# Kernel optimization log

Hardware: AMD Instinct MI355X
Metric: run time of the kernel (lower is better)

Reference implementation:

```python
import jax, jax.numpy as jnp
import numpy as np

B, T_IN, F, U = 4096, 256, 32, 64
OUT_STEPS = 24


def _lstm_step(x, h, c, W, R, b):
    # Keras LSTMCell: gates z = x@W + h@R + b, split as [i, f, g, o]
    z = x @ W + h @ R + b  # [B, 4U]
    i, f, g, o = jnp.split(z, 4, axis=-1)
    i = jax.nn.sigmoid(i)
    f = jax.nn.sigmoid(f)
    g = jnp.tanh(g)
    o = jax.nn.sigmoid(o)
    c_new = f * c + i * g
    h_new = o * jnp.tanh(c_new)
    return h_new, c_new


def setup_inputs() -> dict:
    key = jax.random.key(0)
    ks = jax.random.split(key, 9)
    s_in = 1.0 / np.sqrt(F)
    s_hid = 1.0 / np.sqrt(U)
    return {
        "inputs": jax.random.normal(ks[0], (B, T_IN, F), jnp.float32),
        "W1": jax.random.normal(ks[1], (F, 4 * U), jnp.float32) * s_in,
        "U1": jax.random.normal(ks[2], (U, 4 * U), jnp.float32) * s_hid,
        "b1": jnp.zeros((4 * U,), jnp.float32),
        "W2": jax.random.normal(ks[3], (F, 4 * U), jnp.float32) * s_in,
        "U2": jax.random.normal(ks[4], (U, 4 * U), jnp.float32) * s_hid,
        "b2": jnp.zeros((4 * U,), jnp.float32),
        "Wd": jax.random.normal(ks[5], (U, F), jnp.float32) * s_hid,
        "bd": jnp.zeros((F,), jnp.float32),
    }


def reference(inputs, W1, U1, b1, W2, U2, b2, Wd, bd):
    batch = inputs.shape[0]
    units = U1.shape[0]
    h0 = jnp.zeros((batch, units), inputs.dtype)
    c0 = jnp.zeros((batch, units), inputs.dtype)

    # ---- warmup: run lstm_cell_warmup over the input sequence ----
    def warm_step(carry, x_t):
        h, c = carry
        h, c = _lstm_step(x_t, h, c, W1, U1, b1)
        return (h, c), None

    (h, c), _ = jax.lax.scan(warm_step, (h0, c0), jnp.swapaxes(inputs, 0, 1))
    pred0 = h @ Wd + bd  # [B, F]

    def dec_step(carry, _):
        pred, h, c = carry
        h, c = _lstm_step(pred, h, c, W2, U2, b2)
        pred = h @ Wd + bd
        return (pred, h, c), pred

    _, preds_rest = jax.lax.scan(dec_step, (pred0, h, c), None, length=OUT_STEPS - 1)
    preds = jnp.concatenate([pred0[None], preds_rest], axis=0)  # [T_out, B, F]
    return jnp.transpose(preds, (1, 0, 2))  # [B, T_out, F]
```

## Files before the change

kernel.cpp:

```cpp
#include <hip/hip_runtime.h>
#include <math.h>

#define T_STEPS 256
#define Fdim 32
#define Udim 64
#define G4 256
#define OUT_STEPS 24
#define ROWS 16
#define NBLK 256
#define NTHR 512
#define HBS 72
#define CHUNK 16
#define NCHUNK 16
#define LOG2E 1.4426950408889634f

typedef __attribute__((ext_vector_type(8))) short short8;
typedef __attribute__((ext_vector_type(4))) float f32x4;

__device__ __forceinline__ short f2bf(float f) {
    union { float f; unsigned u; } v; v.f = f;
    unsigned r = v.u + 0x7FFFu + ((v.u >> 16) & 1u);
    return (short)(r >> 16);
}
__device__ __forceinline__ float bf2f(short s) {
    union { unsigned u; float f; } v; v.u = ((unsigned)(unsigned short)s) << 16;
    return v.f;
}
__device__ __forceinline__ float frcp(float v) { return __builtin_amdgcn_rcpf(v); }
__device__ __forceinline__ float fexp2(float v) { return __builtin_amdgcn_exp2f(v); }

__device__ __forceinline__ unsigned pkbf(float lo, float hi) {
    unsigned r;
    asm("v_cvt_pk_bf16_f32 %0, %1, %2" : "=v"(r) : "v"(lo), "v"(hi));
    return r;
}

__device__ __forceinline__ float cell_h(const f32x4 a, float& cst) {
    float A  = fexp2(-a[0]);
    float Bv = fexp2(a[2]);
    float rf = frcp(1.0f + fexp2(-a[1]));
    float ig = (Bv - 1.0f) * frcp((1.0f + A) * (1.0f + Bv));
    cst = fmaf(cst, rf, ig);
    float C  = fexp2(-a[3]);
    float D  = fexp2(2.0f * LOG2E * cst);
    return (D - 1.0f) * frcp((1.0f + C) * (1.0f + D));
}

#define BAR() asm volatile("s_waitcnt lgkmcnt(0)\n\ts_barrier" ::: "memory")

#define MFMA __builtin_amdgcn_mfma_f32_16x16x32_bf16

__global__ __launch_bounds__(NTHR, 2)
void lstm_v10(const float* __restrict__ x,
              const float* __restrict__ W1, const float* __restrict__ U1, const float* __restrict__ b1,
              const float* __restrict__ W2, const float* __restrict__ U2, const float* __restrict__ b2,
              const float* __restrict__ Wd, const float* __restrict__ bd,
              float* __restrict__ out)
{
    __shared__ __align__(16) short hb[2][ROWS][HBS];
    __shared__ __align__(16) short xs[CHUNK][ROWS][HBS];

    const int tid = threadIdx.x;
    const int l   = tid & 63;
    const int w   = tid >> 6;
    const int q   = l >> 4;
    const int m   = l & 15;
    const int brow = blockIdx.x * ROWS;

    const int f4  = tid & 7;
    const int tt  = (tid >> 3) & 15;
    const int xr0 = tid >> 7;
    float4 pf[4];
#pragma unroll
    for (int i = 0; i < 4; ++i)
        pf[i] = *(const float4*)&x[((size_t)(brow + xr0 + 4 * i) * T_STEPS + tt) * Fdim + f4 * 4];

    short8 wa1[2][3], wa2[2][3];
    f32x4 bs1[2], bs2[2];
#pragma unroll
    for (int nt = 0; nt < 2; ++nt) {
        const int unit_a = w * 8 + (m >> 2) * 2 + nt;
        const int gate_a = m & 3;
        const int col = gate_a * 64 + unit_a;
        const float sA = (gate_a == 2) ? 2.0f * LOG2E : LOG2E;
#pragma unroll
        for (int kt = 0; kt < 3; ++kt) {
            short8 fa, fb;
#pragma unroll
            for (int j = 0; j < 8; ++j) {
                const int k = kt * 32 + q * 8 + j;
                float v1 = (k < Udim) ? U1[k * G4 + col] : W1[(k - Udim) * G4 + col];
                float v2 = (k < Udim) ? U2[k * G4 + col] : W2[(k - Udim) * G4 + col];
                fa[j] = f2bf(v1 * sA);
                fb[j] = f2bf(v2 * sA);
            }
            wa1[nt][kt] = fa;
            wa2[nt][kt] = fb;
        }
        const int unit_d = w * 8 + q * 2 + nt;
#pragma unroll
        for (int g = 0; g < 4; ++g) {
            const float sD = (g == 2) ? 2.0f * LOG2E : LOG2E;
            bs1[nt][g] = b1[g * 64 + unit_d] * sD;
            bs2[nt][g] = b2[g * 64 + unit_d] * sD;
        }
    }

    short8 wdh[2], wdlo[2];
    f32x4 bdC;
    {
        const int wsel = (w < 2) ? w : 0;
#pragma unroll
        for (int kt = 0; kt < 2; ++kt) {
            short8 fh, fl;
#pragma unroll
            for (int j = 0; j < 8; ++j) {
                const float v = Wd[(kt * 32 + q * 8 + j) * Fdim + 16 * wsel + m];
                const short hi = f2bf(v);
                fh[j] = hi;
                fl[j] = f2bf(v - bf2f(hi));
            }
            wdh[kt] = fh;
            wdlo[kt] = fl;
        }
#pragma unroll
        for (int g = 0; g < 4; ++g) bdC[g] = bd[16 * wsel + q * 4 + g];
    }

    const int hw = w * 8 + q * 2;
    for (int idx = tid; idx < 2 * ROWS * HBS; idx += NTHR) ((short*)hb)[idx] = 0;
    float cst[2] = {0.f, 0.f};

    for (int c = 0; c < NCHUNK; ++c) {
#pragma unroll
        for (int i = 0; i < 4; ++i) {
            uint2 pk;
            pk.x = pkbf(pf[i].x, pf[i].y);
            pk.y = pkbf(pf[i].z, pf[i].w);
            *(uint2*)&xs[tt][xr0 + 4 * i][f4 * 4] = pk;
        }
        if (c + 1 < NCHUNK) {
#pragma unroll
            for (int i = 0; i < 4; ++i)
                pf[i] = *(const float4*)&x[((size_t)(brow + xr0 + 4 * i) * T_STEPS + ((c + 1) * CHUNK + tt)) * Fdim + f4 * 4];
        }
        BAR();

        short8 xf[CHUNK];
#pragma unroll
        for (int t = 0; t < CHUNK; ++t)
            xf[t] = *(const short8*)&xs[t][m][q * 8];

#pragma unroll
        for (int t2 = 0; t2 < CHUNK; ++t2) {
            const int p = t2 & 1;

            const short8 b0  = *(const short8*)&hb[p][m][q * 8];
            const short8 b1v = *(const short8*)&hb[p][m][32 + q * 8];

            f32x4 a0 = MFMA(wa1[0][2], xf[t2], bs1[0], 0, 0, 0);
            f32x4 a1 = MFMA(wa1[1][2], xf[t2], bs1[1], 0, 0, 0);
            a0 = MFMA(wa1[0][0], b0, a0, 0, 0, 0);
            a1 = MFMA(wa1[1][0], b0, a1, 0, 0, 0);
            a0 = MFMA(wa1[0][1], b1v, a0, 0, 0, 0);
            a1 = MFMA(wa1[1][1], b1v, a1, 0, 0, 0);

            const float h0 = cell_h(a0, cst[0]);
            const float h1 = cell_h(a1, cst[1]);
            *(unsigned*)&hb[1 - p][m][hw] = pkbf(h0, h1);
            BAR();
        }
    }

    short8 b0p = *(const short8*)&hb[0][m][q * 8];
    short8 b1p = *(const short8*)&hb[0][m][32 + q * 8];
    if (w < 2) {
        f32x4 pz = MFMA(wdh[0], b0p, bdC, 0, 0, 0);
        pz = MFMA(wdh[1], b1p, pz, 0, 0, 0);
        pz = MFMA(wdlo[0], b0p, pz, 0, 0, 0);
        pz = MFMA(wdlo[1], b1p, pz, 0, 0, 0);
        *(f32x4*)&out[(size_t)(brow + m) * (OUT_STEPS * Fdim) + 16 * w + q * 4] = pz;
        uint2 fp;
        fp.x = pkbf(pz[0], pz[1]);
        fp.y = pkbf(pz[2], pz[3]);
        *(uint2*)&xs[0][m][16 * w + q * 4] = fp;
    }
    BAR();

    int dp = 0;
    for (int s = 1; s < OUT_STEPS; ++s) {
        const short8 b2v = *(const short8*)&xs[0][m][q * 8];

        f32x4 a0 = MFMA(wa2[0][0], b0p, bs2[0], 0, 0, 0);
        f32x4 a1 = MFMA(wa2[1][0], b0p, bs2[1], 0, 0, 0);
        a0 = MFMA(wa2[0][1], b1p, a0, 0, 0, 0);
        a1 = MFMA(wa2[1][1], b1p, a1, 0, 0, 0);
        a0 = MFMA(wa2[0][2], b2v, a0, 0, 0, 0);
        a1 = MFMA(wa2[1][2], b2v, a1, 0, 0, 0);

        const float h0 = cell_h(a0, cst[0]);
        const float h1 = cell_h(a1, cst[1]);
        *(unsigned*)&hb[1 - dp][m][hw] = pkbf(h0, h1);
        BAR();

        b0p = *(const short8*)&hb[1 - dp][m][q * 8];
        b1p = *(const short8*)&hb[1 - dp][m][32 + q * 8];
        if (w < 2) {
            f32x4 pz = MFMA(wdh[0], b0p, bdC, 0, 0, 0);
            pz = MFMA(wdh[1], b1p, pz, 0, 0, 0);
            pz = MFMA(wdlo[0], b0p, pz, 0, 0, 0);
            pz = MFMA(wdlo[1], b1p, pz, 0, 0, 0);
            *(f32x4*)&out[(size_t)(brow + m) * (OUT_STEPS * Fdim) + s * Fdim + 16 * w + q * 4] = pz;
            uint2 fp;
            fp.x = pkbf(pz[0], pz[1]);
            fp.y = pkbf(pz[2], pz[3]);
            *(uint2*)&xs[0][m][16 * w + q * 4] = fp;
        }
        BAR();
        dp = 1 - dp;
    }
}

extern "C" void kernel_launch(void* const* d_in, const int* in_sizes, int n_in,
                              void* d_out, int out_size, void* d_ws, size_t ws_size,
                              hipStream_t stream) {
    (void)in_sizes; (void)n_in; (void)out_size; (void)d_ws; (void)ws_size;
    const float* x  = (const float*)d_in[0];
    const float* W1 = (const float*)d_in[1];
    const float* U1 = (const float*)d_in[2];
    const float* b1 = (const float*)d_in[3];
    const float* W2 = (const float*)d_in[4];
    const float* U2 = (const float*)d_in[5];
    const float* b2 = (const float*)d_in[6];
    const float* Wd = (const float*)d_in[7];
    const float* bd = (const float*)d_in[8];
    float* out = (float*)d_out;

    lstm_v10<<<dim3(NBLK), dim3(NTHR), 0, stream>>>(
        x, W1, U1, b1, W2, U2, b2, Wd, bd, out);
}
```

Before: 277.5 us.

## Fold dense projection into decoder weights and hoist input MFMAs out of recurrence

The decoder feeds pred = h@Wd + bd back into the cell, so the kernel folds it in algebraically: U2' = U2 + Wd@W2 and b2' = b2 + bd@W2. Each decode step then needs only the recurrent MFMAs, and the dense projection runs off the critical path with one barrier per step instead of two. The warmup input-projection MFMAs for a whole chunk are computed ahead of the recurrent loop, which shortens the serial per-step dependency chain. CHUNK is halved to 8 to limit register pressure from the precomputed accumulators. The folded weights are rounded to bf16, which changes numerics slightly, and each thread does extra setup FMAs to build them.

```diff
diff --git a/kernel.cpp b/kernel.cpp
--- a/kernel.cpp
+++ b/kernel.cpp
@@ -10,8 +10,8 @@
 #define NBLK 256
 #define NTHR 512
 #define HBS 72
-#define CHUNK 16
-#define NCHUNK 16
+#define CHUNK 8
+#define NCHUNK 32
 #define LOG2E 1.4426950408889634f
 
 typedef __attribute__((ext_vector_type(8))) short short8;
@@ -51,7 +51,7 @@
 #define MFMA __builtin_amdgcn_mfma_f32_16x16x32_bf16
 
 __global__ __launch_bounds__(NTHR, 2)
-void lstm_v10(const float* __restrict__ x,
+void lstm_v11(const float* __restrict__ x,
               const float* __restrict__ W1, const float* __restrict__ U1, const float* __restrict__ b1,
               const float* __restrict__ W2, const float* __restrict__ U2, const float* __restrict__ b2,
               const float* __restrict__ Wd, const float* __restrict__ bd,
@@ -67,16 +67,16 @@
     const int m   = l & 15;
     const int brow = blockIdx.x * ROWS;
 
-    const int f4  = tid & 7;
-    const int tt  = (tid >> 3) & 15;
-    const int xr0 = tid >> 7;
-    float4 pf[4];
-#pragma unroll
-    for (int i = 0; i < 4; ++i)
-        pf[i] = *(const float4*)&x[((size_t)(brow + xr0 + 4 * i) * T_STEPS + tt) * Fdim + f4 * 4];
-
-    short8 wa1[2][3], wa2[2][3];
-    f32x4 bs1[2], bs2[2];
+    const int scol = tid & 7;
+    const int sstp = (tid >> 3) & 7;
+    const int srow = tid >> 6;
+    float4 pf[2];
+#pragma unroll
+    for (int i = 0; i < 2; ++i)
+        pf[i] = *(const float4*)&x[((size_t)(brow + srow + 8 * i) * T_STEPS + sstp) * Fdim + scol * 4];
+
+    short8 wa1[2][3];
+    f32x4 bs1[2];
 #pragma unroll
     for (int nt = 0; nt < 2; ++nt) {
         const int unit_a = w * 8 + (m >> 2) * 2 + nt;
@@ -85,24 +85,55 @@
         const float sA = (gate_a == 2) ? 2.0f * LOG2E : LOG2E;
 #pragma unroll
         for (int kt = 0; kt < 3; ++kt) {
-            short8 fa, fb;
+            short8 fa;
 #pragma unroll
             for (int j = 0; j < 8; ++j) {
                 const int k = kt * 32 + q * 8 + j;
-                float v1 = (k < Udim) ? U1[k * G4 + col] : W1[(k - Udim) * G4 + col];
-                float v2 = (k < Udim) ? U2[k * G4 + col] : W2[(k - Udim) * G4 + col];
-                fa[j] = f2bf(v1 * sA);
-                fb[j] = f2bf(v2 * sA);
+                fa[j] = f2bf(((k < Udim) ? U1[k * G4 + col] : W1[(k - Udim) * G4 + col]) * sA);
             }
             wa1[nt][kt] = fa;
-            wa2[nt][kt] = fb;
         }
         const int unit_d = w * 8 + q * 2 + nt;
 #pragma unroll
         for (int g = 0; g < 4; ++g) {
             const float sD = (g == 2) ? 2.0f * LOG2E : LOG2E;
             bs1[nt][g] = b1[g * 64 + unit_d] * sD;
-            bs2[nt][g] = b2[g * 64 + unit_d] * sD;
+        }
+    }
+
+    short8 wa2[2][2];
+    f32x4 bs2[2];
+#pragma unroll
+    for (int nt = 0; nt < 2; ++nt) {
+        const int unit_a = w * 8 + (m >> 2) * 2 + nt;
+        const int gate_a = m & 3;
+        const int col = gate_a * 64 + unit_a;
+        const float sA = (gate_a == 2) ? 2.0f * LOG2E : LOG2E;
+        float w2c[32];
+#pragma unroll
+        for (int f = 0; f < 32; ++f) w2c[f] = W2[f * G4 + col];
+#pragma unroll
+        for (int kt = 0; kt < 2; ++kt) {
+            short8 fb;
+#pragma unroll
+            for (int j = 0; j < 8; ++j) {
+                const int k = kt * 32 + q * 8 + j;
+                float v = U2[k * G4 + col];
+#pragma unroll
+                for (int f = 0; f < 32; ++f) v = fmaf(Wd[k * Fdim + f], w2c[f], v);
+                fb[j] = f2bf(v * sA);
+            }
+            wa2[nt][kt] = fb;
+        }
+        const int unit_d = w * 8 + q * 2 + nt;
+#pragma unroll
+        for (int g = 0; g < 4; ++g) {
+            const float sD = (g == 2) ? 2.0f * LOG2E : LOG2E;
+            const int cb = g * 64 + unit_d;
+            float bv = b2[cb];
+#pragma unroll
+            for (int f = 0; f < 32; ++f) bv = fmaf(bd[f], W2[f * G4 + cb], bv);
+            bs2[nt][g] = bv * sD;
         }
     }
 
@@ -133,23 +164,26 @@
 
     for (int c = 0; c < NCHUNK; ++c) {
 #pragma unroll
-        for (int i = 0; i < 4; ++i) {
+        for (int i = 0; i < 2; ++i) {
             uint2 pk;
             pk.x = pkbf(pf[i].x, pf[i].y);
             pk.y = pkbf(pf[i].z, pf[i].w);
-            *(uint2*)&xs[tt][xr0 + 4 * i][f4 * 4] = pk;
+            *(uint2*)&xs[sstp][srow + 8 * i][scol * 4] = pk;
         }
         if (c + 1 < NCHUNK) {
 #pragma unroll
-            for (int i = 0; i < 4; ++i)
-                pf[i] = *(const float4*)&x[((size_t)(brow + xr0 + 4 * i) * T_STEPS + ((c + 1) * CHUNK + tt)) * Fdim + f4 * 4];
+            for (int i = 0; i < 2; ++i)
+                pf[i] = *(const float4*)&x[((size_t)(brow + srow + 8 * i) * T_STEPS + ((c + 1) * CHUNK + sstp)) * Fdim + scol * 4];
         }
         BAR();
 
-        short8 xf[CHUNK];
-#pragma unroll
-        for (int t = 0; t < CHUNK; ++t)
-            xf[t] = *(const short8*)&xs[t][m][q * 8];
+        f32x4 zx[CHUNK][2];
+#pragma unroll
+        for (int t = 0; t < CHUNK; ++t) {
+            const short8 xf = *(const short8*)&xs[t][m][q * 8];
+            zx[t][0] = MFMA(wa1[0][2], xf, bs1[0], 0, 0, 0);
+            zx[t][1] = MFMA(wa1[1][2], xf, bs1[1], 0, 0, 0);
+        }
 
 #pragma unroll
         for (int t2 = 0; t2 < CHUNK; ++t2) {
@@ -158,10 +192,8 @@
             const short8 b0  = *(const short8*)&hb[p][m][q * 8];
             const short8 b1v = *(const short8*)&hb[p][m][32 + q * 8];
 
-            f32x4 a0 = MFMA(wa1[0][2], xf[t2], bs1[0], 0, 0, 0);
-            f32x4 a1 = MFMA(wa1[1][2], xf[t2], bs1[1], 0, 0, 0);
-            a0 = MFMA(wa1[0][0], b0, a0, 0, 0, 0);
-            a1 = MFMA(wa1[1][0], b0, a1, 0, 0, 0);
+            f32x4 a0 = MFMA(wa1[0][0], b0, zx[t2][0], 0, 0, 0);
+            f32x4 a1 = MFMA(wa1[1][0], b0, zx[t2][1], 0, 0, 0);
             a0 = MFMA(wa1[0][1], b1v, a0, 0, 0, 0);
             a1 = MFMA(wa1[1][1], b1v, a1, 0, 0, 0);
 
@@ -172,52 +204,40 @@
         }
     }
 
-    short8 b0p = *(const short8*)&hb[0][m][q * 8];
-    short8 b1p = *(const short8*)&hb[0][m][32 + q * 8];
-    if (w < 2) {
-        f32x4 pz = MFMA(wdh[0], b0p, bdC, 0, 0, 0);
-        pz = MFMA(wdh[1], b1p, pz, 0, 0, 0);
-        pz = MFMA(wdlo[0], b0p, pz, 0, 0, 0);
-        pz = MFMA(wdlo[1], b1p, pz, 0, 0, 0);
-        *(f32x4*)&out[(size_t)(brow + m) * (OUT_STEPS * Fdim) + 16 * w + q * 4] = pz;
-        uint2 fp;
-        fp.x = pkbf(pz[0], pz[1]);
-        fp.y = pkbf(pz[2], pz[3]);
-        *(uint2*)&xs[0][m][16 * w + q * 4] = fp;
-    }
-    BAR();
-
     int dp = 0;
     for (int s = 1; s < OUT_STEPS; ++s) {
-        const short8 b2v = *(const short8*)&xs[0][m][q * 8];
+        const short8 b0p = *(const short8*)&hb[dp][m][q * 8];
+        const short8 b1p = *(const short8*)&hb[dp][m][32 + q * 8];
 
         f32x4 a0 = MFMA(wa2[0][0], b0p, bs2[0], 0, 0, 0);
         f32x4 a1 = MFMA(wa2[1][0], b0p, bs2[1], 0, 0, 0);
         a0 = MFMA(wa2[0][1], b1p, a0, 0, 0, 0);
         a1 = MFMA(wa2[1][1], b1p, a1, 0, 0, 0);
-        a0 = MFMA(wa2[0][2], b2v, a0, 0, 0, 0);
-        a1 = MFMA(wa2[1][2], b2v, a1, 0, 0, 0);
 
         const float h0 = cell_h(a0, cst[0]);
         const float h1 = cell_h(a1, cst[1]);
         *(unsigned*)&hb[1 - dp][m][hw] = pkbf(h0, h1);
-        BAR();
-
-        b0p = *(const short8*)&hb[1 - dp][m][q * 8];
-        b1p = *(const short8*)&hb[1 - dp][m][32 + q * 8];
+
         if (w < 2) {
             f32x4 pz = MFMA(wdh[0], b0p, bdC, 0, 0, 0);
             pz = MFMA(wdh[1], b1p, pz, 0, 0, 0);
             pz = MFMA(wdlo[0], b0p, pz, 0, 0, 0);
             pz = MFMA(wdlo[1], b1p, pz, 0, 0, 0);
-            *(f32x4*)&out[(size_t)(brow + m) * (OUT_STEPS * Fdim) + s * Fdim + 16 * w + q * 4] = pz;
-            uint2 fp;
-            fp.x = pkbf(pz[0], pz[1]);
-            fp.y = pkbf(pz[2], pz[3]);
-            *(uint2*)&xs[0][m][16 * w + q * 4] = fp;
+            *(f32x4*)&out[(size_t)(brow + m) * (OUT_STEPS * Fdim) + (s - 1) * Fdim + 16 * w + q * 4] = pz;
         }
         BAR();
         dp = 1 - dp;
+    }
+    {
+        const short8 b0p = *(const short8*)&hb[dp][m][q * 8];
+        const short8 b1p = *(const short8*)&hb[dp][m][32 + q * 8];
+        if (w < 2) {
+            f32x4 pz = MFMA(wdh[0], b0p, bdC, 0, 0, 0);
+            pz = MFMA(wdh[1], b1p, pz, 0, 0, 0);
+            pz = MFMA(wdlo[0], b0p, pz, 0, 0, 0);
+            pz = MFMA(wdlo[1], b1p, pz, 0, 0, 0);
+            *(f32x4*)&out[(size_t)(brow + m) * (OUT_STEPS * Fdim) + (OUT_STEPS - 1) * Fdim + 16 * w + q * 4] = pz;
+        }
     }
 }
 
@@ -236,6 +256,6 @@
     const float* bd = (const float*)d_in[8];
     float* out = (float*)d_out;
 
-    lstm_v10<<<dim3(NBLK), dim3(NTHR), 0, stream>>>(
+    lstm_v11<<<dim3(NBLK), dim3(NTHR), 0, stream>>>(
         x, W1, U1, b1, W2, U2, b2, Wd, bd, out);
 }
```

Measured after the change: 480.9 us. 1.73x slower.
